# Optimization experiments

Measured on AMD Instinct MI355X. Metric: run time of the kernel, lower is better.

The kernel has to match this reference:

```python
import jax, jax.numpy as jnp
import numpy as np

N, NFEAT, NHID, E, P, STEPS = 100000, 256, 128, 3200000, 200000, 5
EPS = 1e-6


def _p(key, shape, scale=0.05):
    return (jax.random.normal(key, shape, dtype=jnp.float32) * scale)


def setup_inputs() -> dict:
    key = jax.random.key(0)
    ks = jax.random.split(key, 32)
    inp = {
        "inputs": jax.random.normal(ks[0], (N, NFEAT), dtype=jnp.float32),
        "edge_row": jnp.sort(jax.random.randint(ks[1], (E,), 0, N, dtype=jnp.int32)),
        "edge_col": jax.random.randint(ks[2], (E,), 0, N, dtype=jnp.int32),
        "edge_w": jax.random.uniform(ks[3], (E,), dtype=jnp.float32),
        "x_idx": jax.random.randint(ks[4], (P,), 0, N, dtype=jnp.int32),
        "y_idx": jax.random.randint(ks[5], (P,), 0, N, dtype=jnp.int32),
        # input gates: Linear(nfeat, nhid) with bias
        "Wr_in": _p(ks[6], (NFEAT, NHID)), "br_in": _p(ks[7], (NHID,)),
        "Wi_in": _p(ks[8], (NFEAT, NHID)), "bi_in": _p(ks[9], (NHID,)),
        "Wn_in": _p(ks[10], (NFEAT, NHID)), "bn_in": _p(ks[11], (NHID,)),
        # hidden GCN gates: weight_self + weight_neighbor, no bias
        "Hr_self": _p(ks[12], (NHID, NHID)), "Hr_nb": _p(ks[13], (NHID, NHID)),
        "Hi_self": _p(ks[14], (NHID, NHID)), "Hi_nb": _p(ks[15], (NHID, NHID)),
        "Hh_self": _p(ks[16], (NHID, NHID)), "Hh_nb": _p(ks[17], (NHID, NHID)),
        # post-GRU MLP fc1..fc3
        "W1": _p(ks[18], (NHID, NHID)), "b1": _p(ks[19], (NHID,)),
        "W2": _p(ks[20], (NHID, NHID)), "b2": _p(ks[21], (NHID,)),
        "W3": _p(ks[22], (NHID, NHID)), "b3": _p(ks[23], (NHID,)),
        # layernorm
        "gamma": jnp.ones((NHID,), jnp.float32), "beta": jnp.zeros((NHID,), jnp.float32),
        # decoder
        "Wd1": _p(ks[24], (2 * NHID, NHID)), "bd1": _p(ks[25], (NHID,)),
        "Wd2": _p(ks[26], (NHID, 1)), "bd2": _p(ks[27], (1,)),
    }
    return inp


def _spmm(row, col, w, x):
    # sparse [N,N] @ dense [N,D] via gather + segment_sum
    return jax.ops.segment_sum(x[col] * w[:, None], row, num_segments=N)


def _gcn(h, w_self, w_nb, row, col, ew):
    return h @ w_self + _spmm(row, col, ew, h @ w_nb)


def reference(inputs, edge_row, edge_col, edge_w, x_idx, y_idx,
              Wr_in, br_in, Wi_in, bi_in, Wn_in, bn_in,
              Hr_self, Hr_nb, Hi_self, Hi_nb, Hh_self, Hh_nb,
              W1, b1, W2, b2, W3, b3, gamma, beta,
              Wd1, bd1, Wd2, bd2):
    # input-gate projections are loop-invariant
    in_r = inputs @ Wr_in + br_in
    in_i = inputs @ Wi_in + bi_in
    in_n = inputs @ Wn_in + bn_in
    h = jnp.zeros((inputs.shape[0], NHID), dtype=inputs.dtype)
    for _ in range(STEPS):
        r = jax.nn.sigmoid(in_r + _gcn(h, Hr_self, Hr_nb, edge_row, edge_col, edge_w))
        i = jax.nn.sigmoid(in_i + _gcn(h, Hi_self, Hi_nb, edge_row, edge_col, edge_w))
        n = jnp.tanh(in_n + r * _gcn(h, Hh_self, Hh_nb, edge_row, edge_col, edge_w))
        h = (1.0 - i) * n + i * h
    x = jax.nn.relu(h @ W1 + b1)
    x = jax.nn.relu(x @ W2 + b2)
    x = jax.nn.relu(x @ W3 + b3)
    # torch LayerNorm variant: unbiased std, eps added to std (not var)
    mean = jnp.mean(x, axis=-1, keepdims=True)
    std = jnp.std(x, axis=-1, keepdims=True, ddof=1)
    z = gamma * (x - mean) / (std + EPS) + beta
    # MLP decoder on node pairs
    hcat = jnp.concatenate([z[x_idx], z[y_idx]], axis=1)  # [P, 2*nhid]
    d = jax.nn.relu(hcat @ Wd1 + bd1)
    d = jax.nn.sigmoid(d @ Wd2 + bd2)  # [P, 1]
    return d, z
```

## Files before the change

### kernel.cpp

```cpp
#include <hip/hip_runtime.h>
#include <hip/hip_bf16.h>

#define N_NODES 100000
#define NFEAT 256
#define NHID 128
#define NEDGE 3200000
#define NPAIR 200000
#define NSTEPS 5

typedef __attribute__((ext_vector_type(8))) short short8x;
typedef __attribute__((ext_vector_type(4))) float f32x4;

__device__ __forceinline__ float sigmoidf_(float x) {
    return 1.f / (1.f + __expf(-x));
}
__device__ __forceinline__ unsigned short f2bf_bits(float f) {
    union { float f; unsigned int u; } c; c.f = f;
    unsigned int r = (c.u + 0x7FFFu + ((c.u >> 16) & 1u)) >> 16;
    return (unsigned short)r;
}
__device__ __forceinline__ float bf_bits2f(unsigned short b) {
    union { float f; unsigned int u; } c; c.u = ((unsigned int)b) << 16;
    return c.f;
}
__device__ __forceinline__ int swz8(int row, int q) {
    return row * 32 + ((q + (row >> 1)) & 3) * 8;
}

__global__ void build_row_ptr(const int* __restrict__ rows, int E, int N, int* __restrict__ row_ptr) {
    int i = blockIdx.x * blockDim.x + threadIdx.x;
    if (i > N) return;
    int lo = 0, hi = E;
    while (lo < hi) {
        int mid = (lo + hi) >> 1;
        if (rows[mid] < i) lo = mid + 1; else hi = mid;
    }
    row_ptr[i] = lo;
}

__global__ void pack_kmajor(const float* __restrict__ W, int K, int NCsrc,
                            unsigned short* __restrict__ out, int NCtot, int coff, int koff) {
    int idx = blockIdx.x * blockDim.x + threadIdx.x;
    if (idx >= K * NCsrc) return;
    int k = idx / NCsrc, j = idx - k * NCsrc;
    int kg = k + koff;
    out[(size_t)(kg >> 5) * NCtot * 32 + (size_t)(coff + j) * 32 + (kg & 31)] = f2bf_bits(W[idx]);
}

__global__ void pack_bin(const float* __restrict__ br, const float* __restrict__ bi,
                         const float* __restrict__ bn, float* __restrict__ bin) {
    int i = blockIdx.x * blockDim.x + threadIdx.x;
    if (i >= 384) return;
    bin[i] = (i < 128) ? br[i] : (i < 256) ? bi[i - 128] : bn[i - 256];
}

__global__ __launch_bounds__(256) void gru_step0(
    const unsigned short* __restrict__ IN, unsigned short* __restrict__ hbf, int M)
{
    int t = blockIdx.x * 256 + threadIdx.x;
    int row = t >> 4, ch = (t & 15) * 8;
    if (row >= M) return;
    size_t ib = (size_t)row * 384;
    short8x vi = *reinterpret_cast<const short8x*>(IN + ib + 128 + ch);
    short8x vn = *reinterpret_cast<const short8x*>(IN + ib + 256 + ch);
    short8x o;
    #pragma unroll
    for (int j = 0; j < 8; j++) {
        float ii = sigmoidf_(bf_bits2f((unsigned short)vi[j]));
        float nn = tanhf(bf_bits2f((unsigned short)vn[j]));
        o[j] = (short)f2bf_bits((1.f - ii) * nn);
    }
    *reinterpret_cast<short8x*>(hbf + (size_t)row * 128 + ch) = o;
}

#define SPMM_ACC(hv, we) { \
    acc[0] += (we) * bf_bits2f((unsigned short)(hv).x); \
    acc[1] += (we) * bf_bits2f((unsigned short)((hv).x >> 16)); \
    acc[2] += (we) * bf_bits2f((unsigned short)(hv).y); \
    acc[3] += (we) * bf_bits2f((unsigned short)((hv).y >> 16)); \
    acc[4] += (we) * bf_bits2f((unsigned short)(hv).z); \
    acc[5] += (we) * bf_bits2f((unsigned short)((hv).z >> 16)); \
    acc[6] += (we) * bf_bits2f((unsigned short)(hv).w); \
    acc[7] += (we) * bf_bits2f((unsigned short)((hv).w >> 16)); }

__global__ __launch_bounds__(256) void spmm_bf16_ilp(
    const int* __restrict__ row_ptr, const int* __restrict__ col,
    const float* __restrict__ w, const unsigned short* __restrict__ hbf,
    unsigned short* __restrict__ hsbf, int N)
{
    int v = blockIdx.x * 4 + (threadIdx.x >> 6);
    int lane = threadIdx.x & 63;
    int g = lane >> 4;
    int l16 = lane & 15;
    if (v >= N) return;
    int e0 = row_ptr[v], e1 = row_ptr[v + 1];
    float acc[8] = {};
    int e = e0 + g;
    for (; e + 12 < e1; e += 16) {
        int c1 = col[e], c2 = col[e + 4], c3 = col[e + 8], c4 = col[e + 12];
        float w1 = w[e], w2 = w[e + 4], w3 = w[e + 8], w4 = w[e + 12];
        const uint4 h1 = *reinterpret_cast<const uint4*>(hbf + (size_t)c1 * NHID + l16 * 8);
        const uint4 h2 = *reinterpret_cast<const uint4*>(hbf + (size_t)c2 * NHID + l16 * 8);
        const uint4 h3 = *reinterpret_cast<const uint4*>(hbf + (size_t)c3 * NHID + l16 * 8);
        const uint4 h4 = *reinterpret_cast<const uint4*>(hbf + (size_t)c4 * NHID + l16 * 8);
        SPMM_ACC(h1, w1) SPMM_ACC(h2, w2) SPMM_ACC(h3, w3) SPMM_ACC(h4, w4)
    }
    for (; e < e1; e += 4) {
        int cc = col[e];
        float we = w[e];
        const uint4 hv = *reinterpret_cast<const uint4*>(hbf + (size_t)cc * NHID + l16 * 8);
        SPMM_ACC(hv, we)
    }
    #pragma unroll
    for (int q = 0; q < 8; q++) {
        acc[q] += __shfl_xor(acc[q], 16, 64);
        acc[q] += __shfl_xor(acc[q], 32, 64);
    }
    if (g == 0) {
        uint4 o;
        o.x = (unsigned int)f2bf_bits(acc[0]) | ((unsigned int)f2bf_bits(acc[1]) << 16);
        o.y = (unsigned int)f2bf_bits(acc[2]) | ((unsigned int)f2bf_bits(acc[3]) << 16);
        o.z = (unsigned int)f2bf_bits(acc[4]) | ((unsigned int)f2bf_bits(acc[5]) << 16);
        o.w = (unsigned int)f2bf_bits(acc[6]) | ((unsigned int)f2bf_bits(acc[7]) << 16);
        *reinterpret_cast<uint4*>(hsbf + (size_t)v * NHID + l16 * 8) = o;
    }
}

__global__ __launch_bounds__(256, 3) void gate_step_mfma(
    const unsigned short* __restrict__ hsbf, unsigned short* __restrict__ hbf,
    const unsigned short* __restrict__ IN, const unsigned short* __restrict__ WBg, int M)
{
    __shared__ unsigned short As[64 * 32];
    __shared__ unsigned short Bs[384 * 32];

    const int tid = threadIdx.x;
    const int wid = tid >> 6;
    const int lane = tid & 63;
    const int row0 = blockIdx.x * 64;
    const int l15 = lane & 15;
    const int lhi = lane >> 4;

    f32x4 acc[3][2][4] = {};

    const int ar = tid >> 2;
    const int aq = tid & 3;
    const int agr = row0 + ar;

    for (int s = 0; s < 8; s++) {
        {
            short8x va = short8x(0);
            if (agr < M) {
                const unsigned short* src = (s < 4)
                    ? (hbf  + (size_t)agr * 128 + s * 32)
                    : (hsbf + (size_t)agr * 128 + (s - 4) * 32);
                va = *reinterpret_cast<const short8x*>(src + aq * 8);
            }
            *reinterpret_cast<short8x*>(&As[swz8(ar, aq)]) = va;
        }
        {
            const unsigned short* wbs = WBg + (size_t)s * 384 * 32;
            #pragma unroll
            for (int i = 0; i < 6; i++) {
                int id = tid + i * 256;
                int c = id >> 2, q = id & 3;
                short8x vb = *reinterpret_cast<const short8x*>(wbs + id * 8);
                *reinterpret_cast<short8x*>(&Bs[swz8(c, q)]) = vb;
            }
        }
        __syncthreads();

        short8x a[4];
        #pragma unroll
        for (int rb = 0; rb < 4; rb++)
            a[rb] = *reinterpret_cast<const short8x*>(&As[swz8(16 * rb + l15, lhi)]);
        #pragma unroll
        for (int p = 0; p < 3; p++) {
            #pragma unroll
            for (int cb = 0; cb < 2; cb++) {
                int c0 = 128 * p + 32 * wid + 16 * cb + l15;
                short8x b = *reinterpret_cast<const short8x*>(&Bs[swz8(c0, lhi)]);
                #pragma unroll
                for (int rb = 0; rb < 4; rb++)
                    acc[p][cb][rb] = __builtin_amdgcn_mfma_f32_16x16x32_bf16(b, a[rb], acc[p][cb][rb], 0, 0, 0);
            }
        }
        __syncthreads();
    }

    #pragma unroll
    for (int rb = 0; rb < 4; rb++) {
        int row = row0 + 16 * rb + l15;
        if (row >= M) continue;
        size_t ib = (size_t)row * 384;
        size_t ob = (size_t)row * 128;
        #pragma unroll
        for (int cb = 0; cb < 2; cb++) {
            int cq = 32 * wid + 16 * cb + 4 * lhi;
            const ushort4 vr = *reinterpret_cast<const ushort4*>(IN + ib + cq);
            const ushort4 vi = *reinterpret_cast<const ushort4*>(IN + ib + 128 + cq);
            const ushort4 vn = *reinterpret_cast<const ushort4*>(IN + ib + 256 + cq);
            const ushort4 vh = *reinterpret_cast<const ushort4*>(hbf + ob + cq);
            const unsigned short ra[4] = {vr.x, vr.y, vr.z, vr.w};
            const unsigned short ia[4] = {vi.x, vi.y, vi.z, vi.w};
            const unsigned short na[4] = {vn.x, vn.y, vn.z, vn.w};
            const unsigned short ha[4] = {vh.x, vh.y, vh.z, vh.w};
            unsigned short oa[4];
            #pragma unroll
            for (int j = 0; j < 4; j++) {
                float g_r = acc[0][cb][rb][j] + bf_bits2f(ra[j]);
                float g_i = acc[1][cb][rb][j] + bf_bits2f(ia[j]);
                float rr = sigmoidf_(g_r);
                float gi = sigmoidf_(g_i);
                float nn = tanhf(bf_bits2f(na[j]) + rr * acc[2][cb][rb][j]);
                oa[j] = f2bf_bits((1.f - gi) * nn + gi * bf_bits2f(ha[j]));
            }
            ushort4 st; st.x = oa[0]; st.y = oa[1]; st.z = oa[2]; st.w = oa[3];
            *reinterpret_cast<ushort4*>(hbf + ob + cq) = st;
        }
    }
}

template<int K, int NC, bool F32IN, bool RELU, bool BF16OUT>
__global__ __launch_bounds__(256, 2) void mfma_gemm(
    const void* __restrict__ Xv, const unsigned short* __restrict__ WBx,
    const float* __restrict__ bias, void* __restrict__ C, int M)
{
    constexpr int KS = K / 32;
    constexpr int BI = NC / 64;
    constexpr int NCW = NC / 4;
    constexpr int CB = NCW / 16;
    __shared__ unsigned short As[64 * 32];
    __shared__ unsigned short Bs[NC * 32];

    const int tid = threadIdx.x;
    const int wid = tid >> 6;
    const int lane = tid & 63;
    const int l15 = lane & 15;
    const int lhi = lane >> 4;
    const int row0 = blockIdx.x * 64;

    f32x4 acc[CB][4] = {};

    const int ar = tid >> 2;
    const int aq = tid & 3;
    const int agr = row0 + ar;

    for (int s = 0; s < KS; s++) {
        {
            short8x va = short8x(0);
            if (agr < M) {
                if (F32IN) {
                    const float* src = (const float*)Xv + (size_t)agr * K + s * 32 + aq * 8;
                    const float4 f0 = *reinterpret_cast<const float4*>(src);
                    const float4 f1 = *reinterpret_cast<const float4*>(src + 4);
                    va[0] = (short)f2bf_bits(f0.x); va[1] = (short)f2bf_bits(f0.y);
                    va[2] = (short)f2bf_bits(f0.z); va[3] = (short)f2bf_bits(f0.w);
                    va[4] = (short)f2bf_bits(f1.x); va[5] = (short)f2bf_bits(f1.y);
                    va[6] = (short)f2bf_bits(f1.z); va[7] = (short)f2bf_bits(f1.w);
                } else {
                    va = *reinterpret_cast<const short8x*>(
                        (const unsigned short*)Xv + (size_t)agr * K + s * 32 + aq * 8);
                }
            }
            *reinterpret_cast<short8x*>(&As[swz8(ar, aq)]) = va;
        }
        {
            const unsigned short* wbs = WBx + (size_t)s * NC * 32;
            #pragma unroll
            for (int i = 0; i < BI; i++) {
                int id = tid + i * 256;
                int c = id >> 2, q = id & 3;
                short8x vb = *reinterpret_cast<const short8x*>(wbs + id * 8);
                *reinterpret_cast<short8x*>(&Bs[swz8(c, q)]) = vb;
            }
        }
        __syncthreads();

        short8x a[4];
        #pragma unroll
        for (int rb = 0; rb < 4; rb++)
            a[rb] = *reinterpret_cast<const short8x*>(&As[swz8(16 * rb + l15, lhi)]);
        #pragma unroll
        for (int cb = 0; cb < CB; cb++) {
            int c0 = NCW * wid + 16 * cb + l15;
            short8x b = *reinterpret_cast<const short8x*>(&Bs[swz8(c0, lhi)]);
            #pragma unroll
            for (int rb = 0; rb < 4; rb++)
                acc[cb][rb] = __builtin_amdgcn_mfma_f32_16x16x32_bf16(b, a[rb], acc[cb][rb], 0, 0, 0);
        }
        __syncthreads();
    }

    #pragma unroll
    for (int rb = 0; rb < 4; rb++) {
        int row = row0 + 16 * rb + l15;
        if (row >= M) continue;
        #pragma unroll
        for (int cb = 0; cb < CB; cb++) {
            int cq = NCW * wid + 16 * cb + 4 * lhi;
            float4 bv = make_float4(0.f, 0.f, 0.f, 0.f);
            if (bias) bv = *reinterpret_cast<const float4*>(bias + cq);
            const float bva[4] = {bv.x, bv.y, bv.z, bv.w};
            float o[4];
            #pragma unroll
            for (int j = 0; j < 4; j++) {
                float v = acc[cb][rb][j] + bva[j];
                if (RELU) v = fmaxf(v, 0.f);
                o[j] = v;
            }
            if (BF16OUT) {
                ushort4 st;
                st.x = f2bf_bits(o[0]); st.y = f2bf_bits(o[1]);
                st.z = f2bf_bits(o[2]); st.w = f2bf_bits(o[3]);
                *reinterpret_cast<ushort4*>((unsigned short*)C + (size_t)row * NC + cq) = st;
            } else {
                float4 st; st.x = o[0]; st.y = o[1]; st.z = o[2]; st.w = o[3];
                *reinterpret_cast<float4*>((float*)C + (size_t)row * NC + cq) = st;
            }
        }
    }
}

#define XT_STRIDE 136
__global__ __launch_bounds__(256, 2) void mlp_tail(
    const unsigned short* __restrict__ hbf,
    const unsigned short* __restrict__ WB1, const unsigned short* __restrict__ WB2,
    const unsigned short* __restrict__ WB3, const unsigned short* __restrict__ WBd,
    const float* __restrict__ b1, const float* __restrict__ b2, const float* __restrict__ b3,
    const float* __restrict__ gamma, const float* __restrict__ beta,
    float* __restrict__ out_z, unsigned short* __restrict__ UV, int M)
{
    __shared__ unsigned short As[64 * 32];
    __shared__ unsigned short Bs[256 * 32];
    __shared__ unsigned short xT[64 * XT_STRIDE];

    const int tid = threadIdx.x;
    const int wid = tid >> 6;
    const int lane = tid & 63;
    const int l15 = lane & 15;
    const int lhi = lane >> 4;
    const int row0 = blockIdx.x * 64;
    const int ar = tid >> 2;
    const int aq = tid & 3;

    #pragma unroll
    for (int i = 0; i < 4; i++) {
        int id = tid + i * 256;
        int r = id >> 4, ch = id & 15;
        short8x v = short8x(0);
        if (row0 + r < M)
            v = *reinterpret_cast<const short8x*>(hbf + (size_t)(row0 + r) * 128 + ch * 8);
        *reinterpret_cast<short8x*>(&xT[r * XT_STRIDE + ch * 8]) = v;
    }
    __syncthreads();

    const unsigned short* WLs[3] = {WB1, WB2, WB3};
    const float* bLs[3] = {b1, b2, b3};
    for (int L = 0; L < 3; L++) {
        f32x4 acc[2][4] = {};
        for (int s = 0; s < 4; s++) {
            {
                short8x va = *reinterpret_cast<const short8x*>(&xT[ar * XT_STRIDE + s * 32 + aq * 8]);
                *reinterpret_cast<short8x*>(&As[swz8(ar, aq)]) = va;
            }
            {
                const unsigned short* wbs = WLs[L] + (size_t)s * 128 * 32;
                #pragma unroll
                for (int i = 0; i < 2; i++) {
                    int id = tid + i * 256;
                    int c = id >> 2, q = id & 3;
                    short8x vb = *reinterpret_cast<const short8x*>(wbs + id * 8);
                    *reinterpret_cast<short8x*>(&Bs[swz8(c, q)]) = vb;
                }
            }
            __syncthreads();
            short8x a[4];
            #pragma unroll
            for (int rb = 0; rb < 4; rb++)
                a[rb] = *reinterpret_cast<const short8x*>(&As[swz8(16 * rb + l15, lhi)]);
            #pragma unroll
            for (int cb = 0; cb < 2; cb++) {
                int c0 = 32 * wid + 16 * cb + l15;
                short8x b = *reinterpret_cast<const short8x*>(&Bs[swz8(c0, lhi)]);
                #pragma unroll
                for (int rb = 0; rb < 4; rb++)
                    acc[cb][rb] = __builtin_amdgcn_mfma_f32_16x16x32_bf16(b, a[rb], acc[cb][rb], 0, 0, 0);
            }
            __syncthreads();
        }
        #pragma unroll
        for (int rb = 0; rb < 4; rb++) {
            int r = 16 * rb + l15;
            #pragma unroll
            for (int cb = 0; cb < 2; cb++) {
                int cq = 32 * wid + 16 * cb + 4 * lhi;
                const float4 bv = *reinterpret_cast<const float4*>(bLs[L] + cq);
                const float bva[4] = {bv.x, bv.y, bv.z, bv.w};
                ushort4 st;
                unsigned short* o = (unsigned short*)&st;
                #pragma unroll
                for (int j = 0; j < 4; j++)
                    o[j] = f2bf_bits(fmaxf(acc[cb][rb][j] + bva[j], 0.f));
                *reinterpret_cast<ushort4*>(&xT[r * XT_STRIDE + cq]) = st;
            }
        }
        __syncthreads();
    }

    {
        int r = tid >> 2;
        int grp = tid & 3;
        int c0 = grp * 32;
        float xv[32];
        #pragma unroll
        for (int k = 0; k < 4; k++) {
            short8x v = *reinterpret_cast<const short8x*>(&xT[r * XT_STRIDE + c0 + k * 8]);
            #pragma unroll
            for (int j = 0; j < 8; j++) xv[k * 8 + j] = bf_bits2f((unsigned short)v[j]);
        }
        float s = 0.f;
        #pragma unroll
        for (int q = 0; q < 32; q++) s += xv[q];
        s += __shfl_xor(s, 1, 64);
        s += __shfl_xor(s, 2, 64);
        float mean = s * (1.f / 128.f);
        float vs = 0.f;
        #pragma unroll
        for (int q = 0; q < 32; q++) { float d = xv[q] - mean; vs += d * d; }
        vs += __shfl_xor(vs, 1, 64);
        vs += __shfl_xor(vs, 2, 64);
        float inv = 1.f / (sqrtf(vs / 127.f) + 1e-6f);
        int grow = row0 + r;
        #pragma unroll
        for (int k = 0; k < 4; k++) {
            const float4 gm = *reinterpret_cast<const float4*>(gamma + c0 + k * 8);
            const float4 gm2 = *reinterpret_cast<const float4*>(gamma + c0 + k * 8 + 4);
            const float4 bt = *reinterpret_cast<const float4*>(beta + c0 + k * 8);
            const float4 bt2 = *reinterpret_cast<const float4*>(beta + c0 + k * 8 + 4);
            const float gms[8] = {gm.x, gm.y, gm.z, gm.w, gm2.x, gm2.y, gm2.z, gm2.w};
            const float bts[8] = {bt.x, bt.y, bt.z, bt.w, bt2.x, bt2.y, bt2.z, bt2.w};
            float z[8];
            short8x zb;
            #pragma unroll
            for (int j = 0; j < 8; j++) {
                z[j] = gms[j] * (xv[k * 8 + j] - mean) * inv + bts[j];
                zb[j] = (short)f2bf_bits(z[j]);
            }
            *reinterpret_cast<short8x*>(&xT[r * XT_STRIDE + c0 + k * 8]) = zb;
            if (grow < M) {
                float4 z0 = make_float4(z[0], z[1], z[2], z[3]);
                float4 z1 = make_float4(z[4], z[5], z[6], z[7]);
                *reinterpret_cast<float4*>(out_z + (size_t)grow * 128 + c0 + k * 8) = z0;
                *reinterpret_cast<float4*>(out_z + (size_t)grow * 128 + c0 + k * 8 + 4) = z1;
            }
        }
    }
    __syncthreads();

    {
        f32x4 acc[4][4] = {};
        for (int s = 0; s < 4; s++) {
            {
                short8x va = *reinterpret_cast<const short8x*>(&xT[ar * XT_STRIDE + s * 32 + aq * 8]);
                *reinterpret_cast<short8x*>(&As[swz8(ar, aq)]) = va;
            }
            {
                const unsigned short* wbs = WBd + (size_t)s * 256 * 32;
                #pragma unroll
                for (int i = 0; i < 4; i++) {
                    int id = tid + i * 256;
                    int c = id >> 2, q = id & 3;
                    short8x vb = *reinterpret_cast<const short8x*>(wbs + id * 8);
                    *reinterpret_cast<short8x*>(&Bs[swz8(c, q)]) = vb;
                }
            }
            __syncthreads();
            short8x a[4];
            #pragma unroll
            for (int rb = 0; rb < 4; rb++)
                a[rb] = *reinterpret_cast<const short8x*>(&As[swz8(16 * rb + l15, lhi)]);
            #pragma unroll
            for (int cb = 0; cb < 4; cb++) {
                int c0 = 64 * wid + 16 * cb + l15;
                short8x b = *reinterpret_cast<const short8x*>(&Bs[swz8(c0, lhi)]);
                #pragma unroll
                for (int rb = 0; rb < 4; rb++)
                    acc[cb][rb] = __builtin_amdgcn_mfma_f32_16x16x32_bf16(b, a[rb], acc[cb][rb], 0, 0, 0);
            }
            __syncthreads();
        }
        #pragma unroll
        for (int rb = 0; rb < 4; rb++) {
            int row = row0 + 16 * rb + l15;
            if (row >= M) continue;
            #pragma unroll
            for (int cb = 0; cb < 4; cb++) {
                int cq = 64 * wid + 16 * cb + 4 * lhi;
                ushort4 st;
                st.x = f2bf_bits(acc[cb][rb][0]); st.y = f2bf_bits(acc[cb][rb][1]);
                st.z = f2bf_bits(acc[cb][rb][2]); st.w = f2bf_bits(acc[cb][rb][3]);
                *reinterpret_cast<ushort4*>(UV + (size_t)row * 256 + cq) = st;
            }
        }
    }
}

__global__ __launch_bounds__(256) void decoder_pairs(
    const unsigned short* __restrict__ UV,
    const int* __restrict__ xi, const int* __restrict__ yi,
    const float* __restrict__ bd1, const float* __restrict__ Wd2,
    const float* __restrict__ bd2, float* __restrict__ dout, int P)
{
    __shared__ float b1s[128], w2s[128];
    if (threadIdx.x < 128) {
        b1s[threadIdx.x] = bd1[threadIdx.x];
        w2s[threadIdx.x] = Wd2[threadIdx.x];
    }
    __syncthreads();
    int p = blockIdx.x * 256 + threadIdx.x;
    if (p >= P) return;
    const unsigned short* ur = UV + (size_t)xi[p] * 256;
    const unsigned short* vr = UV + (size_t)yi[p] * 256 + 128;
    float part = 0.f;
    #pragma unroll
    for (int j0 = 0; j0 < 128; j0 += 8) {
        const uint4 ua = *reinterpret_cast<const uint4*>(ur + j0);
        const uint4 va = *reinterpret_cast<const uint4*>(vr + j0);
        float uf[8], vf[8];
        uf[0] = bf_bits2f((unsigned short)ua.x); uf[1] = bf_bits2f((unsigned short)(ua.x >> 16));
        uf[2] = bf_bits2f((unsigned short)ua.y); uf[3] = bf_bits2f((unsigned short)(ua.y >> 16));
        uf[4] = bf_bits2f((unsigned short)ua.z); uf[5] = bf_bits2f((unsigned short)(ua.z >> 16));
        uf[6] = bf_bits2f((unsigned short)ua.w); uf[7] = bf_bits2f((unsigned short)(ua.w >> 16));
        vf[0] = bf_bits2f((unsigned short)va.x); vf[1] = bf_bits2f((unsigned short)(va.x >> 16));
        vf[2] = bf_bits2f((unsigned short)va.y); vf[3] = bf_bits2f((unsigned short)(va.y >> 16));
        vf[4] = bf_bits2f((unsigned short)va.z); vf[5] = bf_bits2f((unsigned short)(va.z >> 16));
        vf[6] = bf_bits2f((unsigned short)va.w); vf[7] = bf_bits2f((unsigned short)(va.w >> 16));
        #pragma unroll
        for (int q = 0; q < 8; q++) {
            float t = uf[q] + vf[q] + b1s[j0 + q];
            part += fmaxf(t, 0.f) * w2s[j0 + q];
        }
    }
    dout[p] = sigmoidf_(part + bd2[0]);
}

extern "C" void kernel_launch(void* const* d_in, const int* in_sizes, int n_in,
                              void* d_out, int out_size, void* d_ws, size_t ws_size,
                              hipStream_t stream) {
    const float* inputs = (const float*)d_in[0];
    const int* edge_row = (const int*)d_in[1];
    const int* edge_col = (const int*)d_in[2];
    const float* edge_w = (const float*)d_in[3];
    const int* x_idx = (const int*)d_in[4];
    const int* y_idx = (const int*)d_in[5];
    const float* Wr_in = (const float*)d_in[6];  const float* br_in = (const float*)d_in[7];
    const float* Wi_in = (const float*)d_in[8];  const float* bi_in = (const float*)d_in[9];
    const float* Wn_in = (const float*)d_in[10]; const float* bn_in = (const float*)d_in[11];
    const float* Hr_self = (const float*)d_in[12]; const float* Hr_nb = (const float*)d_in[13];
    const float* Hi_self = (const float*)d_in[14]; const float* Hi_nb = (const float*)d_in[15];
    const float* Hh_self = (const float*)d_in[16]; const float* Hh_nb = (const float*)d_in[17];
    const float* W1 = (const float*)d_in[18]; const float* b1 = (const float*)d_in[19];
    const float* W2 = (const float*)d_in[20]; const float* b2 = (const float*)d_in[21];
    const float* W3 = (const float*)d_in[22]; const float* b3 = (const float*)d_in[23];
    const float* gamma = (const float*)d_in[24]; const float* beta = (const float*)d_in[25];
    const float* Wd1 = (const float*)d_in[26]; const float* bd1 = (const float*)d_in[27];
    const float* Wd2 = (const float*)d_in[28]; const float* bd2 = (const float*)d_in[29];

    float* out_d = (float*)d_out;
    float* out_z = ((float*)d_out) + NPAIR;

    char* base = (char*)d_ws;
    size_t off = 0;
    auto take = [&](size_t bytes) { void* p = base + off; off = (off + bytes + 255) & ~(size_t)255; return p; };
    int*            row_ptr = (int*)           take((size_t)(N_NODES + 1) * 4);
    unsigned short* WBg     = (unsigned short*)take((size_t)8 * 384 * 32 * 2);
    unsigned short* WBin    = (unsigned short*)take((size_t)8 * 384 * 32 * 2);
    unsigned short* WB1     = (unsigned short*)take((size_t)4 * 128 * 32 * 2);
    unsigned short* WB2     = (unsigned short*)take((size_t)4 * 128 * 32 * 2);
    unsigned short* WB3     = (unsigned short*)take((size_t)4 * 128 * 32 * 2);
    unsigned short* WBd     = (unsigned short*)take((size_t)4 * 256 * 32 * 2);
    float*          bin     = (float*)         take(384 * 4);
    unsigned short* IN      = (unsigned short*)take((size_t)N_NODES * 384 * 2);
    unsigned short* hbf     = (unsigned short*)take((size_t)N_NODES * NHID * 2);
    unsigned short* hsbf    = (unsigned short*)take((size_t)N_NODES * NHID * 2);
    if (off > ws_size) return;

    build_row_ptr<<<(N_NODES + 256) / 256, 256, 0, stream>>>(edge_row, NEDGE, N_NODES, row_ptr);
    pack_kmajor<<<64, 256, 0, stream>>>(Hr_self, 128, 128, WBg, 384, 0, 0);
    pack_kmajor<<<64, 256, 0, stream>>>(Hi_self, 128, 128, WBg, 384, 128, 0);
    pack_kmajor<<<64, 256, 0, stream>>>(Hh_self, 128, 128, WBg, 384, 256, 0);
    pack_kmajor<<<64, 256, 0, stream>>>(Hr_nb,   128, 128, WBg, 384, 0, 128);
    pack_kmajor<<<64, 256, 0, stream>>>(Hi_nb,   128, 128, WBg, 384, 128, 128);
    pack_kmajor<<<64, 256, 0, stream>>>(Hh_nb,   128, 128, WBg, 384, 256, 128);
    pack_kmajor<<<128, 256, 0, stream>>>(Wr_in, 256, 128, WBin, 384, 0, 0);
    pack_kmajor<<<128, 256, 0, stream>>>(Wi_in, 256, 128, WBin, 384, 128, 0);
    pack_kmajor<<<128, 256, 0, stream>>>(Wn_in, 256, 128, WBin, 384, 256, 0);
    pack_kmajor<<<64, 256, 0, stream>>>(W1, 128, 128, WB1, 128, 0, 0);
    pack_kmajor<<<64, 256, 0, stream>>>(W2, 128, 128, WB2, 128, 0, 0);
    pack_kmajor<<<64, 256, 0, stream>>>(W3, 128, 128, WB3, 128, 0, 0);
    pack_kmajor<<<64, 256, 0, stream>>>(Wd1,             128, 128, WBd, 256, 0, 0);
    pack_kmajor<<<64, 256, 0, stream>>>(Wd1 + 128 * 128, 128, 128, WBd, 256, 128, 0);
    pack_bin<<<2, 256, 0, stream>>>(br_in, bi_in, bn_in, bin);
    int grid64 = (N_NODES + 63) / 64;
    mfma_gemm<256, 384, true, false, true><<<grid64, 256, 0, stream>>>(inputs, WBin, bin, IN, N_NODES);
    gru_step0<<<(N_NODES * 16 + 255) / 256, 256, 0, stream>>>(IN, hbf, N_NODES);
    for (int s = 1; s < NSTEPS; s++) {
        spmm_bf16_ilp<<<(N_NODES + 3) / 4, 256, 0, stream>>>(row_ptr, edge_col, edge_w, hbf, hsbf, N_NODES);
        gate_step_mfma<<<grid64, 256, 0, stream>>>(hsbf, hbf, IN, WBg, N_NODES);
    }
    unsigned short* UV = IN;
    mlp_tail<<<grid64, 256, 0, stream>>>(hbf, WB1, WB2, WB3, WBd, b1, b2, b3,
                                         gamma, beta, out_z, UV, N_NODES);
    decoder_pairs<<<(NPAIR + 255) / 256, 256, 0, stream>>>(
        UV, x_idx, y_idx, bd1, Wd2, bd2, out_d, NPAIR);
}
```

Measured before the change: 998.7 us.

## Enlarge gate-step GEMM tile to 128 rows and batch weight packing into one launch

The fused gate-step MFMA kernel now processes 128 rows per block with 512 threads (8 waves), each wave owning 16 columns per gate across 8 row blocks. The 384x32 weight slab staged in shared memory per K-step is therefore reused across twice as many rows, which halves weight traffic into LDS. The trade-off is less occupancy and fewer blocks per step. Separately, the fourteen weight-packing launches are merged into one 2D-grid launch driven by a descriptor struct, cutting launch overhead.

```diff
diff --git a/kernel.cpp b/kernel.cpp
--- a/kernel.cpp
+++ b/kernel.cpp
@@ -38,13 +38,21 @@
     row_ptr[i] = lo;
 }
 
-__global__ void pack_kmajor(const float* __restrict__ W, int K, int NCsrc,
-                            unsigned short* __restrict__ out, int NCtot, int coff, int koff) {
-    int idx = blockIdx.x * blockDim.x + threadIdx.x;
-    if (idx >= K * NCsrc) return;
-    int k = idx / NCsrc, j = idx - k * NCsrc;
-    int kg = k + koff;
-    out[(size_t)(kg >> 5) * NCtot * 32 + (size_t)(coff + j) * 32 + (kg & 31)] = f2bf_bits(W[idx]);
+struct PackDesc {
+    const float* src;
+    unsigned short* dst;
+    int K, NCsrc, NCtot, coff, koff;
+};
+struct PackDescs { PackDesc d[14]; };
+
+__global__ void pack_all(PackDescs P) {
+    const PackDesc pd = P.d[blockIdx.y];
+    int idx = blockIdx.x * 256 + threadIdx.x;
+    if (idx >= pd.K * pd.NCsrc) return;
+    int k = idx / pd.NCsrc, j = idx - k * pd.NCsrc;
+    int kg = k + pd.koff;
+    pd.dst[(size_t)(kg >> 5) * pd.NCtot * 32 + (size_t)(pd.coff + j) * 32 + (kg & 31)] =
+        f2bf_bits(pd.src[idx]);
 }
 
 __global__ void pack_bin(const float* __restrict__ br, const float* __restrict__ bi,
@@ -126,21 +134,21 @@
     }
 }
 
-__global__ __launch_bounds__(256, 3) void gate_step_mfma(
+__global__ __launch_bounds__(512, 2) void gate_step_mfma(
     const unsigned short* __restrict__ hsbf, unsigned short* __restrict__ hbf,
     const unsigned short* __restrict__ IN, const unsigned short* __restrict__ WBg, int M)
 {
-    __shared__ unsigned short As[64 * 32];
+    __shared__ unsigned short As[128 * 32];
     __shared__ unsigned short Bs[384 * 32];
 
     const int tid = threadIdx.x;
     const int wid = tid >> 6;
     const int lane = tid & 63;
-    const int row0 = blockIdx.x * 64;
+    const int row0 = blockIdx.x * 128;
     const int l15 = lane & 15;
     const int lhi = lane >> 4;
 
-    f32x4 acc[3][2][4] = {};
+    f32x4 acc[3][8] = {};
 
     const int ar = tid >> 2;
     const int aq = tid & 3;
@@ -160,8 +168,8 @@
         {
             const unsigned short* wbs = WBg + (size_t)s * 384 * 32;
             #pragma unroll
-            for (int i = 0; i < 6; i++) {
-                int id = tid + i * 256;
+            for (int i = 0; i < 3; i++) {
+                int id = tid + i * 512;
                 int c = id >> 2, q = id & 3;
                 short8x vb = *reinterpret_cast<const short8x*>(wbs + id * 8);
                 *reinterpret_cast<short8x*>(&Bs[swz8(c, q)]) = vb;
@@ -169,54 +177,48 @@
         }
         __syncthreads();
 
-        short8x a[4];
-        #pragma unroll
-        for (int rb = 0; rb < 4; rb++)
+        short8x a[8];
+        #pragma unroll
+        for (int rb = 0; rb < 8; rb++)
             a[rb] = *reinterpret_cast<const short8x*>(&As[swz8(16 * rb + l15, lhi)]);
         #pragma unroll
         for (int p = 0; p < 3; p++) {
-            #pragma unroll
-            for (int cb = 0; cb < 2; cb++) {
-                int c0 = 128 * p + 32 * wid + 16 * cb + l15;
-                short8x b = *reinterpret_cast<const short8x*>(&Bs[swz8(c0, lhi)]);
-                #pragma unroll
-                for (int rb = 0; rb < 4; rb++)
-                    acc[p][cb][rb] = __builtin_amdgcn_mfma_f32_16x16x32_bf16(b, a[rb], acc[p][cb][rb], 0, 0, 0);
-            }
+            int c0 = 128 * p + 16 * wid + l15;
+            short8x b = *reinterpret_cast<const short8x*>(&Bs[swz8(c0, lhi)]);
+            #pragma unroll
+            for (int rb = 0; rb < 8; rb++)
+                acc[p][rb] = __builtin_amdgcn_mfma_f32_16x16x32_bf16(b, a[rb], acc[p][rb], 0, 0, 0);
         }
         __syncthreads();
     }
 
+    const int cq = 16 * wid + 4 * lhi;
     #pragma unroll
-    for (int rb = 0; rb < 4; rb++) {
+    for (int rb = 0; rb < 8; rb++) {
         int row = row0 + 16 * rb + l15;
         if (row >= M) continue;
         size_t ib = (size_t)row * 384;
         size_t ob = (size_t)row * 128;
-        #pragma unroll
-        for (int cb = 0; cb < 2; cb++) {
-            int cq = 32 * wid + 16 * cb + 4 * lhi;
-            const ushort4 vr = *reinterpret_cast<const ushort4*>(IN + ib + cq);
-            const ushort4 vi = *reinterpret_cast<const ushort4*>(IN + ib + 128 + cq);
-            const ushort4 vn = *reinterpret_cast<const ushort4*>(IN + ib + 256 + cq);
-            const ushort4 vh = *reinterpret_cast<const ushort4*>(hbf + ob + cq);
-            const unsigned short ra[4] = {vr.x, vr.y, vr.z, vr.w};
-            const unsigned short ia[4] = {vi.x, vi.y, vi.z, vi.w};
-            const unsigned short na[4] = {vn.x, vn.y, vn.z, vn.w};
-            const unsigned short ha[4] = {vh.x, vh.y, vh.z, vh.w};
-            unsigned short oa[4];
-            #pragma unroll
-            for (int j = 0; j < 4; j++) {
-                float g_r = acc[0][cb][rb][j] + bf_bits2f(ra[j]);
-                float g_i = acc[1][cb][rb][j] + bf_bits2f(ia[j]);
-                float rr = sigmoidf_(g_r);
-                float gi = sigmoidf_(g_i);
-                float nn = tanhf(bf_bits2f(na[j]) + rr * acc[2][cb][rb][j]);
-                oa[j] = f2bf_bits((1.f - gi) * nn + gi * bf_bits2f(ha[j]));
-            }
-            ushort4 st; st.x = oa[0]; st.y = oa[1]; st.z = oa[2]; st.w = oa[3];
-            *reinterpret_cast<ushort4*>(hbf + ob + cq) = st;
-        }
+        const ushort4 vr = *reinterpret_cast<const ushort4*>(IN + ib + cq);
+        const ushort4 vi = *reinterpret_cast<const ushort4*>(IN + ib + 128 + cq);
+        const ushort4 vn = *reinterpret_cast<const ushort4*>(IN + ib + 256 + cq);
+        const ushort4 vh = *reinterpret_cast<const ushort4*>(hbf + ob + cq);
+        const unsigned short ra[4] = {vr.x, vr.y, vr.z, vr.w};
+        const unsigned short ia[4] = {vi.x, vi.y, vi.z, vi.w};
+        const unsigned short na[4] = {vn.x, vn.y, vn.z, vn.w};
+        const unsigned short ha[4] = {vh.x, vh.y, vh.z, vh.w};
+        unsigned short oa[4];
+        #pragma unroll
+        for (int j = 0; j < 4; j++) {
+            float g_r = acc[0][rb][j] + bf_bits2f(ra[j]);
+            float g_i = acc[1][rb][j] + bf_bits2f(ia[j]);
+            float rr = sigmoidf_(g_r);
+            float gi = sigmoidf_(g_i);
+            float nn = tanhf(bf_bits2f(na[j]) + rr * acc[2][rb][j]);
+            oa[j] = f2bf_bits((1.f - gi) * nn + gi * bf_bits2f(ha[j]));
+        }
+        ushort4 st; st.x = oa[0]; st.y = oa[1]; st.z = oa[2]; st.w = oa[3];
+        *reinterpret_cast<ushort4*>(hbf + ob + cq) = st;
     }
 }
 
@@ -586,27 +588,37 @@
     if (off > ws_size) return;
 
     build_row_ptr<<<(N_NODES + 256) / 256, 256, 0, stream>>>(edge_row, NEDGE, N_NODES, row_ptr);
-    pack_kmajor<<<64, 256, 0, stream>>>(Hr_self, 128, 128, WBg, 384, 0, 0);
-    pack_kmajor<<<64, 256, 0, stream>>>(Hi_self, 128, 128, WBg, 384, 128, 0);
-    pack_kmajor<<<64, 256, 0, stream>>>(Hh_self, 128, 128, WBg, 384, 256, 0);
-    pack_kmajor<<<64, 256, 0, stream>>>(Hr_nb,   128, 128, WBg, 384, 0, 128);
-    pack_kmajor<<<64, 256, 0, stream>>>(Hi_nb,   128, 128, WBg, 384, 128, 128);
-    pack_kmajor<<<64, 256, 0, stream>>>(Hh_nb,   128, 128, WBg, 384, 256, 128);
-    pack_kmajor<<<128, 256, 0, stream>>>(Wr_in, 256, 128, WBin, 384, 0, 0);
-    pack_kmajor<<<128, 256, 0, stream>>>(Wi_in, 256, 128, WBin, 384, 128, 0);
-    pack_kmajor<<<128, 256, 0, stream>>>(Wn_in, 256, 128, WBin, 384, 256, 0);
-    pack_kmajor<<<64, 256, 0, stream>>>(W1, 128, 128, WB1, 128, 0, 0);
-    pack_kmajor<<<64, 256, 0, stream>>>(W2, 128, 128, WB2, 128, 0, 0);
-    pack_kmajor<<<64, 256, 0, stream>>>(W3, 128, 128, WB3, 128, 0, 0);
-    pack_kmajor<<<64, 256, 0, stream>>>(Wd1,             128, 128, WBd, 256, 0, 0);
-    pack_kmajor<<<64, 256, 0, stream>>>(Wd1 + 128 * 128, 128, 128, WBd, 256, 128, 0);
+    {
+        PackDescs P;
+        auto set = [&](int i, const float* src, unsigned short* dst, int K, int NCsrc,
+                       int NCtot, int coff, int koff) {
+            P.d[i] = PackDesc{src, dst, K, NCsrc, NCtot, coff, koff};
+        };
+        set(0,  Hr_self, WBg, 128, 128, 384, 0,   0);
+        set(1,  Hi_self, WBg, 128, 128, 384, 128, 0);
+        set(2,  Hh_self, WBg, 128, 128, 384, 256, 0);
+        set(3,  Hr_nb,   WBg, 128, 128, 384, 0,   128);
+        set(4,  Hi_nb,   WBg, 128, 128, 384, 128, 128);
+        set(5,  Hh_nb,   WBg, 128, 128, 384, 256, 128);
+        set(6,  Wr_in,   WBin, 256, 128, 384, 0,   0);
+        set(7,  Wi_in,   WBin, 256, 128, 384, 128, 0);
+        set(8,  Wn_in,   WBin, 256, 128, 384, 256, 0);
+        set(9,  W1,      WB1, 128, 128, 128, 0, 0);
+        set(10, W2,      WB2, 128, 128, 128, 0, 0);
+        set(11, W3,      WB3, 128, 128, 128, 0, 0);
+        set(12, Wd1,             WBd, 128, 128, 256, 0,   0);
+        set(13, Wd1 + 128 * 128, WBd, 128, 128, 256, 128, 0);
+        dim3 pg(128, 14);
+        pack_all<<<pg, 256, 0, stream>>>(P);
+    }
     pack_bin<<<2, 256, 0, stream>>>(br_in, bi_in, bn_in, bin);
     int grid64 = (N_NODES + 63) / 64;
+    int grid128 = (N_NODES + 127) / 128;
     mfma_gemm<256, 384, true, false, true><<<grid64, 256, 0, stream>>>(inputs, WBin, bin, IN, N_NODES);
     gru_step0<<<(N_NODES * 16 + 255) / 256, 256, 0, stream>>>(IN, hbf, N_NODES);
     for (int s = 1; s < NSTEPS; s++) {
         spmm_bf16_ilp<<<(N_NODES + 3) / 4, 256, 0, stream>>>(row_ptr, edge_col, edge_w, hbf, hsbf, N_NODES);
-        gate_step_mfma<<<grid64, 256, 0, stream>>>(hsbf, hbf, IN, WBg, N_NODES);
+        gate_step_mfma<<<grid128, 512, 0, stream>>>(hsbf, hbf, IN, WBg, N_NODES);
     }
     unsigned short* UV = IN;
     mlp_tail<<<grid64, 256, 0, stream>>>(hbf, WB1, WB2, WB3, WBd, b1, b2, b3,
```

Result: faster. 956.5 us (-4.2%).
